# Kernel tuning notes

Measured on AMD Instinct MI355X. Metric: run time of the kernel, lower is better.

Reference implementation:

```python
import jax, jax.numpy as jnp
import numpy as np

B, D, H, G, WR = 8192, 1024, 1024, 2, 64
URANKS = [64, 64]


def setup_inputs() -> dict:
    key = jax.random.key(0)
    ks = jax.random.split(key, 12)
    s = 0.1
    return {
        "x": jax.random.normal(ks[0], (B, D), jnp.float32),
        "h": jax.random.normal(ks[1], (B, H), jnp.float32),
        "c": jax.random.normal(ks[2], (B, H), jnp.float32),
        "dia_x": s * jax.random.normal(ks[3], (1, D), jnp.float32),
        "dia_h": s * jax.random.normal(ks[4], (1, H), jnp.float32),
        "Ux": s * jax.random.normal(ks[5], (D, WR), jnp.float32),
        "Vx": s * jax.random.normal(ks[6], (4 * H, WR), jnp.float32),
        "Uh_0": s * jax.random.normal(ks[7], (G, H // G, URANKS[0]), jnp.float32),
        "Vh_0": s * jax.random.normal(ks[8], (G, URANKS[0], 4 * (H // G)), jnp.float32),
        "Uh_1": s * jax.random.normal(ks[9], (G, H // G, URANKS[1]), jnp.float32),
        "Vh_1": s * jax.random.normal(ks[10], (G, URANKS[1], 4 * (H // G)), jnp.float32),
        "bias_x": jnp.ones((1, 4 * H), jnp.float32),
        "bias_h": jnp.ones((1, 4 * H), jnp.float32),
    }


def reference(x, h, c, dia_x, dia_h, Ux, Vx, Uh_0, Vh_0, Uh_1, Vh_1, bias_x, bias_h):
    Bn, Dn = x.shape
    Hn = h.shape[1]
    g = Uh_0.shape[0]
    Hg = Hn // g
    r0 = Uh_0.shape[2]

    # diagonal (vector-multiplication) paths, x-part zero-padded to hidden width
    vm_x = jnp.pad(dia_x * x, ((0, 0), (0, Hn - Dn)))          # [B, H]
    vm_h = dia_h * h                                           # [B, H]

    # low-rank input projection
    lowered_x = (x @ Ux) @ Vx.T                                # [B, 4H]

    # refined diagonal corrections subtracted from the low-rank outputs
    Vx4 = Vx.reshape(4, Hn, -1)[:, :Dn, :]                     # [4, D, wR]
    coef_x = jnp.sum(Ux[None, :, :] * Vx4, axis=-1)            # [4, D]
    vm_refined_x = jnp.pad(x[:, None, :] * coef_x[None], ((0, 0), (0, 0), (0, Hn - Dn))).reshape(Bn, 4 * Hn)

    Uh0f = Uh_0.reshape(Hn, r0)                                # [H, r0]
    Vh0f = jnp.transpose(Vh_0, (0, 2, 1)).reshape(4 * Hn, r0).reshape(4, Hn, r0)
    coef_h = jnp.sum(Uh0f[None, :, :] * Vh0f, axis=-1)         # [4, H]
    vm_refined_h = (h[:, None, :] * coef_h[None]).reshape(Bn, 4 * Hn)

    gx = lowered_x - vm_refined_x + bias_x
    xi, xf, xo, xn = jnp.split(gx, 4, axis=1)

    # grouped low-rank recurrent projection with cyclic group permutation
    hv = h.reshape(Bn, g, Hg)
    Uhs = [Uh_0, Uh_1]
    Vhs = [Vh_0, Vh_1]
    g_h = jnp.zeros((Bn, 4 * Hn), x.dtype)
    for i in range(g):
        idx = np.roll(np.arange(g), -i)                        # static permutation
        hp = hv[:, idx, :]                                     # [B, g, H/g]
        t = jnp.einsum('bgn,gnr->bgr', hp, Uhs[i])             # [B, g, r_i]
        t = jnp.einsum('bgr,grm->bgm', t, Vhs[i])              # [B, g, 4H/g]
        g_h = g_h + t.reshape(Bn, 4 * Hn)

    gh = g_h - vm_refined_h + bias_h
    hf, hi, hn, ho = jnp.split(gh, 4, axis=1)                  # note gate order differs from x

    base = vm_x + vm_h
    inputgate = jax.nn.sigmoid(xi + hi + base)
    forgetgate = jax.nn.sigmoid(xf + hf + base)
    outputgate = jax.nn.sigmoid(xo + ho + base)
    newgate = jnp.tanh(xn + hn + base)

    c_next = forgetgate * c + inputgate * newgate
    h_next = outputgate * jnp.tanh(c_next)
    return (h_next, c_next)
```

## Files before the change

### kernel.cpp

```cpp
#include <hip/hip_runtime.h>


typedef _Float16 half8 __attribute__((ext_vector_type(8)));
typedef _Float16 half4v __attribute__((ext_vector_type(4)));
typedef float f32x4 __attribute__((ext_vector_type(4)));

#define WS_U1F   0
#define WS_UH1F  131072
#define WS_W2    393216
#define WS_CX    1966080
#define WS_CH    1982464
#define WS_BB    1998848

__global__ __launch_bounds__(256) void prep_kernel(
    const float* __restrict__ Ux, const float* __restrict__ Vx,
    const float* __restrict__ Uh0, const float* __restrict__ Vh0,
    const float* __restrict__ Uh1, const float* __restrict__ Vh1,
    const float* __restrict__ dia_x, const float* __restrict__ dia_h,
    const float* __restrict__ bias_x, const float* __restrict__ bias_h,
    _Float16* __restrict__ U1f, _Float16* __restrict__ Uh1f,
    _Float16* __restrict__ W2f, float* __restrict__ cx,
    float* __restrict__ ch, float* __restrict__ bb)
{
    int e = blockIdx.x * 256 + threadIdx.x;
    if (e < 8192) {
        int lane = e & 63, ks = (e >> 6) & 31, ct = e >> 11;
        int l15 = lane & 15, quad = lane >> 4;
        half8 v8;
        #pragma unroll
        for (int jj = 0; jj < 8; ++jj) {
            int k = ks * 32 + quad * 8 + jj;
            v8[jj] = (_Float16)Ux[k * 64 + ct * 16 + l15];
        }
        *(half8*)&U1f[(size_t)e * 8] = v8;
    } else if (e < 24576) {
        int t = e - 8192;
        int lane = t & 63, ks = (t >> 6) & 15, ct = (t >> 10) & 3, j = t >> 12;
        int l15 = lane & 15, quad = lane >> 4;
        const float* src = (j & 1) ? Uh1 : Uh0;
        int g = j >> 1;
        half8 v8;
        #pragma unroll
        for (int jj = 0; jj < 8; ++jj) {
            int k = ks * 32 + quad * 8 + jj;
            v8[jj] = (_Float16)src[(g * 512 + k) * 64 + ct * 16 + l15];
        }
        *(half8*)&Uh1f[(size_t)t * 8] = v8;
    } else if (e < 122880) {
        int t = e - 24576;
        int lane = t & 63;
        int ksq  = (t >> 6) % 6;
        int ct   = (t / 384) & 63;
        int g01  = (t / 24576) & 1;
        int s    = t / 49152;
        int l15 = lane & 15, quad = lane >> 4;
        int k = ct * 16 + l15;
        int jx = s * 2 + g01;
        int m = (g01 == 0) ? (1024 + k) : k;
        half8 v8;
        #pragma unroll
        for (int jj = 0; jj < 8; ++jj) {
            int kk = ksq * 32 + quad * 8 + jj;
            int r = kk & 63, sect = kk >> 6;
            float val;
            if (sect == 0)      val = Vx[(jx * 1024 + k) * 64 + r];
            else if (sect == 1) val = Vh0[(s * 64 + r) * 2048 + m];
            else                val = Vh1[(s * 64 + r) * 2048 + m];
            v8[jj] = (_Float16)val;
        }
        *(half8*)&W2f[(size_t)t * 8] = v8;
    } else {
        int t64 = e - 122880;
        int t = t64 >> 6;
        int r = t64 & 63;
        int q = t >> 10; int k = t & 1023;
        int jh = q ^ 1;
        int fh = jh * 1024 + k; int g = fh >> 11; int m = fh & 2047;
        float sx = Ux[k * 64 + r] * Vx[(q * 1024 + k) * 64 + r];
        float sh = Uh0[k * 64 + r] * Vh0[(g * 64 + r) * 2048 + m];
        #pragma unroll
        for (int d = 32; d > 0; d >>= 1) {
            sx += __shfl_xor(sx, d, 64);
            sh += __shfl_xor(sh, d, 64);
        }
        if (r == 0) {
            cx[t] = dia_x[k] - sx;
            ch[t] = dia_h[k] - sh;
            bb[t] = bias_x[q * 1024 + k] + bias_h[jh * 1024 + k];
        }
    }
}

__global__ __launch_bounds__(1024) void fused_kernel(
    const float* __restrict__ x, const float* __restrict__ h,
    const float* __restrict__ c,
    const _Float16* __restrict__ U1f, const _Float16* __restrict__ Uh1f,
    const _Float16* __restrict__ W2f,
    const float* __restrict__ cx, const float* __restrict__ ch,
    const float* __restrict__ bb, float* __restrict__ out)
{
    __shared__ __align__(16) _Float16 Xsh[32][1032];
    __shared__ __align__(16) _Float16 Hsh[32][1032];
    __shared__ __align__(16) _Float16 Tsh[32][328];

    const int tid = threadIdx.x;
    const int w = tid >> 6, l = tid & 63, l15 = l & 15, quad = l >> 4;
    const int b0 = blockIdx.x * 32;
    const size_t rowbase = (size_t)b0 * 1024;

    {
        const float* xs = x + rowbase;
        const float* hs = h + rowbase;
        #pragma unroll
        for (int ii = 0; ii < 8; ++ii) {
            int idx = tid + ii * 1024;
            int row = idx >> 8, c4 = idx & 255;
            f32x4 fx = __builtin_nontemporal_load(
                (const f32x4*)&xs[(size_t)row * 1024 + c4 * 4]);
            f32x4 fh = __builtin_nontemporal_load(
                (const f32x4*)&hs[(size_t)row * 1024 + c4 * 4]);
            half4v px, ph;
            px[0] = (_Float16)fx[0]; px[1] = (_Float16)fx[1];
            px[2] = (_Float16)fx[2]; px[3] = (_Float16)fx[3];
            ph[0] = (_Float16)fh[0]; ph[1] = (_Float16)fh[1];
            ph[2] = (_Float16)fh[2]; ph[3] = (_Float16)fh[3];
            *(half4v*)&Xsh[row][c4 * 4] = px;
            *(half4v*)&Hsh[row][c4 * 4] = ph;
        }
    }
    __syncthreads();

    if (w < 8) {
        int rt = w & 1, ct = w >> 1;
        f32x4 acc = {};
        const _Float16* bp = U1f + ((size_t)(ct * 32) * 64 + l) * 8;
        #pragma unroll
        for (int ks = 0; ks < 32; ++ks) {
            half8 a = *(const half8*)&Xsh[rt * 16 + l15][ks * 32 + quad * 8];
            half8 b = *(const half8*)(bp + (size_t)ks * 512);
            acc = __builtin_amdgcn_mfma_f32_16x16x32_f16(a, b, acc, 0, 0, 0);
        }
        #pragma unroll
        for (int r = 0; r < 4; ++r)
            Tsh[rt * 16 + quad * 4 + r][ct * 16 + l15] = (_Float16)acc[r];
    }
    {
        int pstart = (w < 8) ? w : 8 + (w - 8) * 3;
        int pcnt   = (w < 8) ? 1 : 3;
        for (int ii = 0; ii < 3; ++ii) {
            if (ii >= pcnt) break;
            int p = pstart + ii;
            int j = p >> 3, rem = p & 7, prt = rem >> 2, pct = rem & 3;
            int hoff = (j == 1 || j == 2) ? 512 : 0;
            f32x4 pa = {};
            const _Float16* pb = Uh1f + ((size_t)((j * 4 + pct) * 16) * 64 + l) * 8;
            #pragma unroll
            for (int ks = 0; ks < 16; ++ks) {
                half8 a = *(const half8*)&Hsh[prt * 16 + l15][hoff + ks * 32 + quad * 8];
                half8 b = *(const half8*)(pb + (size_t)ks * 512);
                pa = __builtin_amdgcn_mfma_f32_16x16x32_f16(a, b, pa, 0, 0, 0);
            }
            #pragma unroll
            for (int r = 0; r < 4; ++r)
                Tsh[prt * 16 + quad * 4 + r][64 + j * 64 + pct * 16 + l15] = (_Float16)pa[r];
        }
    }
    __syncthreads();

    const int secIF[3] = {0, 64, 128};
    const int secON[3] = {0, 192, 256};

    float cpref[2][2][4];
    {
        int k0 = w * 16 + l15;
        #pragma unroll
        for (int rt = 0; rt < 2; ++rt)
            #pragma unroll
            for (int r = 0; r < 4; ++r)
                cpref[0][rt][r] = __builtin_nontemporal_load(
                    &c[rowbase + (size_t)(rt * 16 + quad * 4 + r) * 1024 + k0]);
    }

    #pragma unroll
    for (int i = 0; i < 4; ++i) {
        const int ctg = w + 16 * i;
        const int k = ctg * 16 + l15;

        if (i < 3) {
            int kn = k + 256;
            #pragma unroll
            for (int rt = 0; rt < 2; ++rt)
                #pragma unroll
                for (int r = 0; r < 4; ++r)
                    cpref[(i + 1) & 1][rt][r] = __builtin_nontemporal_load(
                        &c[rowbase + (size_t)(rt * 16 + quad * 4 + r) * 1024 + kn]);
        }

        float cxi = cx[k], cxf = cx[1024 + k], cxo = cx[2048 + k], cxn = cx[3072 + k];
        float chi = ch[k], chf = ch[1024 + k], cho = ch[2048 + k], chn = ch[3072 + k];
        float bbi = bb[k], bbf = bb[1024 + k], bbo = bb[2048 + k], bbn = bb[3072 + k];

        const size_t laneoff = (size_t)l * 8;
        const _Float16* bpi = W2f + (size_t)((0 * 64 + ctg) * 6) * 512 + laneoff;
        const _Float16* bpf = W2f + (size_t)((1 * 64 + ctg) * 6) * 512 + laneoff;
        const _Float16* bpo = W2f + (size_t)((2 * 64 + ctg) * 6) * 512 + laneoff;
        const _Float16* bpn = W2f + (size_t)((3 * 64 + ctg) * 6) * 512 + laneoff;

        f32x4 acc[4][2] = {};
        #pragma unroll
        for (int ks = 0; ks < 6; ++ks) {
            half8 bi = *(const half8*)(bpi + (size_t)ks * 512);
            half8 bf = *(const half8*)(bpf + (size_t)ks * 512);
            half8 bo = *(const half8*)(bpo + (size_t)ks * 512);
            half8 bn = *(const half8*)(bpn + (size_t)ks * 512);
            int coff = (ks & 1) * 32 + quad * 8;
            #pragma unroll
            for (int rt = 0; rt < 2; ++rt) {
                half8 aA = *(const half8*)&Tsh[rt * 16 + l15][secIF[ks >> 1] + coff];
                half8 aB = *(const half8*)&Tsh[rt * 16 + l15][secON[ks >> 1] + coff];
                acc[0][rt] = __builtin_amdgcn_mfma_f32_16x16x32_f16(aA, bi, acc[0][rt], 0, 0, 0);
                acc[1][rt] = __builtin_amdgcn_mfma_f32_16x16x32_f16(aA, bf, acc[1][rt], 0, 0, 0);
                acc[2][rt] = __builtin_amdgcn_mfma_f32_16x16x32_f16(aB, bo, acc[2][rt], 0, 0, 0);
                acc[3][rt] = __builtin_amdgcn_mfma_f32_16x16x32_f16(aB, bn, acc[3][rt], 0, 0, 0);
            }
        }

        #pragma unroll
        for (int rt = 0; rt < 2; ++rt) {
            #pragma unroll
            for (int r = 0; r < 4; ++r) {
                int rl = rt * 16 + quad * 4 + r;
                size_t off = rowbase + (size_t)rl * 1024 + k;
                float xv = (float)Xsh[rl][k];
                float hv = (float)Hsh[rl][k];
                float cvv = cpref[i & 1][rt][r];
                float pi = acc[0][rt][r] + xv * cxi + hv * chi + bbi;
                float pf = acc[1][rt][r] + xv * cxf + hv * chf + bbf;
                float po = acc[2][rt][r] + xv * cxo + hv * cho + bbo;
                float pn = acc[3][rt][r] + xv * cxn + hv * chn + bbn;
                float ig = __builtin_amdgcn_rcpf(1.f + __expf(-pi));
                float fg = __builtin_amdgcn_rcpf(1.f + __expf(-pf));
                float og = __builtin_amdgcn_rcpf(1.f + __expf(-po));
                float ng = 1.f - 2.f * __builtin_amdgcn_rcpf(__expf(2.f * pn) + 1.f);
                float cn = fg * cvv + ig * ng;
                float tc = 1.f - 2.f * __builtin_amdgcn_rcpf(__expf(2.f * cn) + 1.f);
                out[off] = og * tc;
                out[(size_t)8388608 + off] = cn;
            }
        }
    }
}

extern "C" void kernel_launch(void* const* d_in, const int* in_sizes, int n_in,
                              void* d_out, int out_size, void* d_ws, size_t ws_size,
                              hipStream_t stream)
{
    const float* x      = (const float*)d_in[0];
    const float* h      = (const float*)d_in[1];
    const float* c      = (const float*)d_in[2];
    const float* dia_x  = (const float*)d_in[3];
    const float* dia_h  = (const float*)d_in[4];
    const float* Ux     = (const float*)d_in[5];
    const float* Vx     = (const float*)d_in[6];
    const float* Uh0    = (const float*)d_in[7];
    const float* Vh0    = (const float*)d_in[8];
    const float* Uh1    = (const float*)d_in[9];
    const float* Vh1    = (const float*)d_in[10];
    const float* bias_x = (const float*)d_in[11];
    const float* bias_h = (const float*)d_in[12];
    float* out = (float*)d_out;

    char* ws = (char*)d_ws;
    _Float16* U1f  = (_Float16*)(ws + WS_U1F);
    _Float16* Uh1f = (_Float16*)(ws + WS_UH1F);
    _Float16* W2f  = (_Float16*)(ws + WS_W2);
    float* cx = (float*)(ws + WS_CX);
    float* ch = (float*)(ws + WS_CH);
    float* bb = (float*)(ws + WS_BB);

    prep_kernel<<<1504, 256, 0, stream>>>(Ux, Vx, Uh0, Vh0, Uh1, Vh1,
                                          dia_x, dia_h, bias_x, bias_h,
                                          U1f, Uh1f, W2f, cx, ch, bb);
    fused_kernel<<<256, 1024, 0, stream>>>(x, h, c, U1f, Uh1f, W2f,
                                           cx, ch, bb, out);
}
```

Measured before the change: 203.2 us.

## Stage Vh transpose through LDS and shrink weight-prep grid

Rewrites the weight-prep kernel. The Vh0/Vh1 parts of the packed W2 layout are now built by dedicated blocks that load rows coalesced, convert to fp16 in shared memory, and write transposed half8 fragments. Previously each thread read strided Vh columns. The diagonal-coefficient reductions now use one thread per output with a serial loop instead of one wave-wide shuffle reduction per output. The grid drops from 1504 blocks to 272, which cuts strided global reads but leaves fewer threads for the serial reductions.

```diff
diff --git a/kernel.cpp b/kernel.cpp
--- a/kernel.cpp
+++ b/kernel.cpp
@@ -22,7 +22,46 @@
     _Float16* __restrict__ W2f, float* __restrict__ cx,
     float* __restrict__ ch, float* __restrict__ bb)
 {
-    int e = blockIdx.x * 256 + threadIdx.x;
+    __shared__ __align__(16) _Float16 Tl[64][260];
+
+    const int tid = threadIdx.x;
+    if (blockIdx.x >= 240) {
+        int bid2 = blockIdx.x - 240;
+        int s = bid2 & 1, i = (bid2 >> 1) & 1, mchunk = bid2 >> 2;
+        const float* Vh = i ? Vh1 : Vh0;
+        #pragma unroll
+        for (int it = 0; it < 16; ++it) {
+            int idx = tid + it * 256;
+            int row = idx >> 6, c4 = idx & 63;
+            f32x4 v = *(const f32x4*)&Vh[(size_t)(s * 64 + row) * 2048
+                                         + mchunk * 256 + c4 * 4];
+            half4v p;
+            p[0] = (_Float16)v[0]; p[1] = (_Float16)v[1];
+            p[2] = (_Float16)v[2]; p[3] = (_Float16)v[3];
+            *(half4v*)&Tl[row][c4 * 4] = p;
+        }
+        __syncthreads();
+        int lane = tid & 63, l15 = lane & 15, quad = lane >> 4;
+        #pragma unroll
+        for (int q = 0; q < 8; ++q) {
+            int combo = (tid >> 6) * 8 + q;
+            int ct_local = combo >> 1, rk = combo & 1;
+            int m_local = ct_local * 16 + l15;
+            int m = mchunk * 256 + m_local;
+            int g01 = (m >= 1024) ? 0 : 1;
+            int ct_global = (m - (1 - g01) * 1024) >> 4;
+            int ksq = 2 + 2 * i + rk;
+            half8 v8;
+            #pragma unroll
+            for (int jj = 0; jj < 8; ++jj)
+                v8[jj] = Tl[rk * 32 + quad * 8 + jj][m_local];
+            size_t t_out = (((size_t)(s * 2 + g01) * 64 + ct_global) * 6 + ksq) * 64 + lane;
+            *(half8*)&W2f[t_out * 8] = v8;
+        }
+        return;
+    }
+
+    int e = blockIdx.x * 256 + tid;
     if (e < 8192) {
         int lane = e & 63, ks = (e >> 6) & 31, ct = e >> 11;
         int l15 = lane & 15, quad = lane >> 4;
@@ -46,48 +85,40 @@
             v8[jj] = (_Float16)src[(g * 512 + k) * 64 + ct * 16 + l15];
         }
         *(half8*)&Uh1f[(size_t)t * 8] = v8;
-    } else if (e < 122880) {
-        int t = e - 24576;
-        int lane = t & 63;
-        int ksq  = (t >> 6) % 6;
-        int ct   = (t / 384) & 63;
-        int g01  = (t / 24576) & 1;
-        int s    = t / 49152;
+    } else if (e < 57344) {
+        int tt = e - 24576;
+        int lane = tt & 63;
+        int ksq2 = (tt >> 6) & 1;
+        int ct   = (tt / 128) & 63;
+        int g01  = (tt / 8192) & 1;
+        int s    = tt / 16384;
         int l15 = lane & 15, quad = lane >> 4;
         int k = ct * 16 + l15;
         int jx = s * 2 + g01;
-        int m = (g01 == 0) ? (1024 + k) : k;
         half8 v8;
         #pragma unroll
         for (int jj = 0; jj < 8; ++jj) {
-            int kk = ksq * 32 + quad * 8 + jj;
-            int r = kk & 63, sect = kk >> 6;
-            float val;
-            if (sect == 0)      val = Vx[(jx * 1024 + k) * 64 + r];
-            else if (sect == 1) val = Vh0[(s * 64 + r) * 2048 + m];
-            else                val = Vh1[(s * 64 + r) * 2048 + m];
-            v8[jj] = (_Float16)val;
-        }
-        *(half8*)&W2f[(size_t)t * 8] = v8;
-    } else {
-        int t64 = e - 122880;
-        int t = t64 >> 6;
-        int r = t64 & 63;
+            int r = ksq2 * 32 + quad * 8 + jj;
+            v8[jj] = (_Float16)Vx[(jx * 1024 + k) * 64 + r];
+        }
+        size_t t_out = (((size_t)(s * 2 + g01) * 64 + ct) * 6 + ksq2) * 64 + lane;
+        *(half8*)&W2f[t_out * 8] = v8;
+    } else if (e < 61440) {
+        int t = e - 57344;
         int q = t >> 10; int k = t & 1023;
         int jh = q ^ 1;
         int fh = jh * 1024 + k; int g = fh >> 11; int m = fh & 2047;
-        float sx = Ux[k * 64 + r] * Vx[(q * 1024 + k) * 64 + r];
-        float sh = Uh0[k * 64 + r] * Vh0[(g * 64 + r) * 2048 + m];
-        #pragma unroll
-        for (int d = 32; d > 0; d >>= 1) {
-            sx += __shfl_xor(sx, d, 64);
-            sh += __shfl_xor(sh, d, 64);
-        }
-        if (r == 0) {
-            cx[t] = dia_x[k] - sx;
-            ch[t] = dia_h[k] - sh;
-            bb[t] = bias_x[q * 1024 + k] + bias_h[jh * 1024 + k];
-        }
+        float sx0 = 0.f, sx1 = 0.f, sh0 = 0.f, sh1 = 0.f;
+        #pragma unroll 4
+        for (int r = 0; r < 64; r += 2) {
+            sx0 += Ux[k * 64 + r]     * Vx[(q * 1024 + k) * 64 + r];
+            sx1 += Ux[k * 64 + r + 1] * Vx[(q * 1024 + k) * 64 + r + 1];
+            sh0 += Uh0[k * 64 + r]     * Vh0[(size_t)(g * 64 + r) * 2048 + m];
+            sh1 += Uh0[k * 64 + r + 1] * Vh0[(size_t)(g * 64 + r + 1) * 2048 + m];
+        }
+        cx[t] = dia_x[k] - (sx0 + sx1);
+        ch[t] = dia_h[k] - (sh0 + sh1);
+        bb[t] = bias_x[q * 1024 + k] + bias_h[jh * 1024 + k];
     }
 }
 
@@ -278,9 +309,9 @@
     float* ch = (float*)(ws + WS_CH);
     float* bb = (float*)(ws + WS_BB);
 
-    prep_kernel<<<1504, 256, 0, stream>>>(Ux, Vx, Uh0, Vh0, Uh1, Vh1,
-                                          dia_x, dia_h, bias_x, bias_h,
-                                          U1f, Uh1f, W2f, cx, ch, bb);
+    prep_kernel<<<272, 256, 0, stream>>>(Ux, Vx, Uh0, Vh0, Uh1, Vh1,
+                                         dia_x, dia_h, bias_x, bias_h,
+                                         U1f, Uh1f, W2f, cx, ch, bb);
     fused_kernel<<<256, 1024, 0, stream>>>(x, h, c, U1f, Uh1f, W2f,
                                            cx, ch, bb, out);
 }
```

Result: slower. 208.0 us (+2.4%).
